# Kernel optimization log

Measured on AMD Instinct MI355X. Metric: run time of the kernel, lower is better.

Reference implementation:

```python
import jax, jax.numpy as jnp
import numpy as np
import math

L = 6          # num_layers
D = 512        # hidden_dim
S = 2048       # seq_len
B = 8          # batch
ODIM = 1       # output_dim
SCALES = (24.0, 720.0)


def setup_inputs() -> dict:
    key = jax.random.key(0)
    ks = jax.random.split(key, 12)
    def n(k, shape, scale=0.02):
        return jax.random.normal(k, shape, dtype=jnp.float32) * scale
    return {
        "z": jax.random.normal(ks[0], (B, S, 1), dtype=jnp.float32),
        "c": jax.random.normal(ks[1], (B, S, 1), dtype=jnp.float32),
        "enc_w": n(ks[2], (D, 2)), "enc_b": jnp.zeros((D,), jnp.float32),
        "beta": jnp.ones((L, len(SCALES)), jnp.float32),
        "wq": n(ks[3], (L, D, D)), "bq": jnp.zeros((L, D), jnp.float32),
        "wk": n(ks[4], (L, D, D)), "bk": jnp.zeros((L, D), jnp.float32),
        "wv": n(ks[5], (L, D, D)), "bv": jnp.zeros((L, D), jnp.float32),
        "ln1_w": jnp.ones((L, D), jnp.float32), "ln1_b": jnp.zeros((L, D), jnp.float32),
        "ln2_w": jnp.ones((L, D), jnp.float32), "ln2_b": jnp.zeros((L, D), jnp.float32),
        "ff1_w": n(ks[6], (L, 4 * D, D)), "ff1_b": jnp.zeros((L, 4 * D), jnp.float32),
        "ff2_w": n(ks[7], (L, D, 4 * D)), "ff2_b": jnp.zeros((L, D), jnp.float32),
        "out_w": n(ks[8], (ODIM, D)), "out_b": jnp.zeros((ODIM,), jnp.float32),
    }


def _ln(x, w, b, eps=1e-5):
    m = jnp.mean(x, axis=-1, keepdims=True)
    v = jnp.var(x, axis=-1, keepdims=True)
    return (x - m) * jax.lax.rsqrt(v + eps) * w + b


def _posenc(seq_len, dim):
    pos = jnp.arange(seq_len, dtype=jnp.float32)[:, None]
    div = jnp.exp(jnp.arange(0, dim, 2, dtype=jnp.float32) * (-(math.log(10000.0) / dim)))
    pe = jnp.zeros((seq_len, dim), jnp.float32)
    pe = pe.at[:, 0::2].set(jnp.sin(pos * div))
    pe = pe.at[:, 1::2].set(jnp.cos(pos * div))
    return pe


def reference(z, c, enc_w, enc_b, beta, wq, bq, wk, bk, wv, bv,
              ln1_w, ln1_b, ln2_w, ln2_b, ff1_w, ff1_b, ff2_w, ff2_b,
              out_w, out_b):
    # SequenceEncoder: cat(z,c) -> Linear(2, D) -> + sinusoidal PE
    x = jnp.concatenate([z, c], axis=-1) @ enc_w.T + enc_b       # [B,S,D]
    seq_len, d = x.shape[1], x.shape[2]
    x = x + _posenc(seq_len, d)[None]
    sqrt_d = math.sqrt(d)

    idx = jnp.arange(seq_len, dtype=jnp.float32)
    dist = jnp.abs(idx[:, None] - idx[None, :])                  # [S,S]

    for l in range(L):
        # pre-norm with ln1 (applied twice in the original code - replicated)
        xn = _ln(x, ln1_w[l], ln1_b[l])
        Q = xn @ wq[l].T + bq[l]
        K = xn @ wk[l].T + bk[l]
        V = xn @ wv[l].T + bv[l]
        attn = jnp.einsum('bid,bjd->bij', Q, K) / sqrt_d          # [B,S,S]
        bias = beta[l, 0] * jnp.cos(2.0 * math.pi * dist / SCALES[0]) \
             + beta[l, 1] * jnp.cos(2.0 * math.pi * dist / SCALES[1])
        probs = jax.nn.softmax(attn + bias, axis=-1)
        att_out = jnp.einsum('bij,bjd->bid', probs, V)
        # original applies layer_norm_1 again to the residual sum
        x = _ln(x + att_out, ln1_w[l], ln1_b[l])
        xn2 = _ln(x, ln2_w[l], ln2_b[l])
        h = jax.nn.relu(xn2 @ ff1_w[l].T + ff1_b[l])
        x = x + h @ ff2_w[l].T + ff2_b[l]

    return x @ out_w.T + out_b                                    # [B,S,ODIM]
```

## Files before the change

### kernel.cpp

```cpp
#include <hip/hip_runtime.h>
#include <math.h>

#define BB 8
#define SS 2048
#define DD 512
#define LL 6
#define FFD 2048

typedef _Float16 half_t;
typedef __attribute__((ext_vector_type(8))) _Float16 half8;
typedef __attribute__((ext_vector_type(4))) _Float16 half4;
typedef __attribute__((ext_vector_type(4))) float f32x4;

enum { EPI_NONE = 0, EPI_RELU = 2, EPI_RES = 3, EPI_ATTN = 4, EPI_QKV = 5, EPI_PV = 6 };

__device__ __forceinline__ void gl_lds16(const void* g, void* l) {
    __builtin_amdgcn_global_load_lds(
        (const __attribute__((address_space(1))) unsigned int*)g,
        (__attribute__((address_space(3))) unsigned int*)l,
        16, 0, 0);
}

__device__ __forceinline__ void blockReduce2(float& a, float& b, float* sm) {
#pragma unroll
    for (int off = 32; off; off >>= 1) {
        a += __shfl_down(a, off);
        b += __shfl_down(b, off);
    }
    int lane = threadIdx.x & 63;
    int w = threadIdx.x >> 6;
    if (lane == 0) { sm[w] = a; sm[4 + w] = b; }
    __syncthreads();
    a = sm[0] + sm[1] + sm[2] + sm[3];
    b = sm[4] + sm[5] + sm[6] + sm[7];
    __syncthreads();
}

__global__ __launch_bounds__(256) void encode_kernel(
    const float* __restrict__ z, const float* __restrict__ c,
    const float* __restrict__ enc_w, const float* __restrict__ enc_b,
    float* __restrict__ x)
{
    int idx = blockIdx.x * 256 + threadIdx.x;
    int d  = idx & (DD - 1);
    int bs = idx >> 9;
    int s  = bs & (SS - 1);
    float v = z[bs] * enc_w[2 * d] + c[bs] * enc_w[2 * d + 1] + enc_b[d];
    float div = expf(-(float)(d & ~1) * (9.210340371976184f / 512.0f));
    float ang = (float)s * div;
    v += (d & 1) ? cosf(ang) : sinf(ang);
    x[idx] = v;
}

__global__ __launch_bounds__(256) void convert_layer_kernel(
    const float* __restrict__ wq, const float* __restrict__ wk,
    const float* __restrict__ wv, const float* __restrict__ f1,
    const float* __restrict__ f2, half_t* __restrict__ wqkv,
    half_t* __restrict__ f1h, half_t* __restrict__ f2h)
{
    const int NQ = DD * DD;
    int i = blockIdx.x * 256 + threadIdx.x;
    if (i < 3 * NQ) {
        int which = i >> 18, j = i & (NQ - 1);
        const float* s = (which == 0) ? wq : (which == 1) ? wk : wv;
        wqkv[i] = (half_t)s[j];
    } else {
        int k = i - 3 * NQ;
        if (k < FFD * DD) f1h[k] = (half_t)f1[k];
        else              f2h[k - FFD * DD] = (half_t)f2[k - FFD * DD];
    }
}

__global__ __launch_bounds__(256) void bias_table_kernel(
    const float* __restrict__ beta, float* __restrict__ tbl)
{
    int i = blockIdx.x * 256 + threadIdx.x;
    int l = i >> 11, d = i & (SS - 1);
    tbl[i] = beta[2 * l] * cosf(0.2617993877991494f * d)
           + beta[2 * l + 1] * cosf(0.008726646259971648f * d);
}

__global__ __launch_bounds__(256) void ln_kernel(
    const float* __restrict__ src, const float* __restrict__ w,
    const float* __restrict__ b, half_t* __restrict__ dst)
{
    __shared__ float sm[8];
    size_t row = blockIdx.x;
    const float* p = src + row * DD;
    int t = threadIdx.x;
    float v0 = p[t], v1 = p[t + 256];
    float s = v0 + v1, sq = v0 * v0 + v1 * v1;
    blockReduce2(s, sq, sm);
    float mean = s * (1.0f / DD);
    float var  = sq * (1.0f / DD) - mean * mean;
    float rs   = rsqrtf(var + 1e-5f);
    dst[row * DD + t]       = (half_t)((v0 - mean) * rs * w[t] + b[t]);
    dst[row * DD + t + 256] = (half_t)((v1 - mean) * rs * w[t + 256] + b[t + 256]);
}

__global__ __launch_bounds__(256) void add_ln_ln_kernel(
    float* __restrict__ x, const half_t* __restrict__ att,
    const float* __restrict__ w1, const float* __restrict__ b1,
    const float* __restrict__ w2, const float* __restrict__ b2,
    half_t* __restrict__ xn)
{
    __shared__ float sm[8];
    size_t row = blockIdx.x;
    int t = threadIdx.x;
    float v0 = x[row * DD + t] + (float)att[row * DD + t];
    float v1 = x[row * DD + t + 256] + (float)att[row * DD + t + 256];
    float s = v0 + v1, sq = v0 * v0 + v1 * v1;
    blockReduce2(s, sq, sm);
    float mean = s * (1.0f / DD);
    float var  = sq * (1.0f / DD) - mean * mean;
    float rs   = rsqrtf(var + 1e-5f);
    float y0 = (v0 - mean) * rs * w1[t] + b1[t];
    float y1 = (v1 - mean) * rs * w1[t + 256] + b1[t + 256];
    x[row * DD + t]       = y0;
    x[row * DD + t + 256] = y1;
    s = y0 + y1; sq = y0 * y0 + y1 * y1;
    blockReduce2(s, sq, sm);
    mean = s * (1.0f / DD);
    var  = sq * (1.0f / DD) - mean * mean;
    rs   = rsqrtf(var + 1e-5f);
    xn[row * DD + t]       = (half_t)((y0 - mean) * rs * w2[t] + b2[t]);
    xn[row * DD + t + 256] = (half_t)((y1 - mean) * rs * w2[t + 256] + b2[t + 256]);
}

template<int MT, int EPI, bool OHALF>
__global__ __launch_bounds__(256) void gemm_mfma(
    const half_t* __restrict__ A, const half_t* __restrict__ W,
    const float* __restrict__ bias, const float* __restrict__ res,
    void* __restrict__ Cp, int N, int K, float alpha,
    long long sA, long long sW, long long sC,
    const float* __restrict__ biasK, const float* __restrict__ biasV,
    half_t* __restrict__ Ck, half_t* __restrict__ Cv)
{
    constexpr int TM = MT / 32;
    constexpr int ABUF = MT * 32;
    constexpr int BBUF = 128 * 32;
    __shared__ __align__(16) half_t As[2 * ABUF];
    __shared__ __align__(16) half_t Bs[2 * BBUF];

    const int z = blockIdx.z;
    A += (size_t)z * sA; W += (size_t)z * sW;
    if (EPI == EPI_PV) res += (size_t)z * SS;
    float*  Cf = (float*)Cp  + (size_t)z * sC;
    half_t* Ch = (half_t*)Cp + (size_t)z * sC;

    const int tid = threadIdx.x;
    const int wv = tid >> 6, ln = tid & 63;
    const int bm = blockIdx.x * MT, bn = blockIdx.y * 128;
    const int wm = (wv & 1) * (MT / 2), wn = (wv >> 1) * 64;

    const int srow = wv * 16 + (ln >> 2);
    const int scol = (ln & 3) * 8;
    const half_t* Ag = A + (size_t)(bm + srow) * K + scol;
    const half_t* Bg = W + (size_t)(bn + srow) * K + scol;

    f32x4 acc[TM][4] = {};
    const int lane15 = ln & 15, quad = ln >> 4;
    const int koff = quad * 8;
    const int nIter = K >> 5;

    {
        char* a = (char*)As + wv * 1024;
        char* b = (char*)Bs + wv * 1024;
        gl_lds16(Ag, a);
        if (MT == 128) gl_lds16(Ag + (size_t)64 * K, a + 4096);
        gl_lds16(Bg, b);
        gl_lds16(Bg + (size_t)64 * K, b + 4096);
    }
    __syncthreads();

    for (int it = 0; it < nIter; ++it) {
        const int cur = it & 1;
        if (it + 1 < nIter) {
            const int k1 = (it + 1) << 5;
            char* a = (char*)As + (cur ^ 1) * (ABUF * 2) + wv * 1024;
            char* b = (char*)Bs + (cur ^ 1) * (BBUF * 2) + wv * 1024;
            gl_lds16(Ag + k1, a);
            if (MT == 128) gl_lds16(Ag + (size_t)64 * K + k1, a + 4096);
            gl_lds16(Bg + k1, b);
            gl_lds16(Bg + (size_t)64 * K + k1, b + 4096);
        }

        const half_t* Ab = As + cur * ABUF;
        const half_t* Bb = Bs + cur * BBUF;
        half8 aF[TM], bF[4];
#pragma unroll
        for (int i = 0; i < TM; ++i)
            aF[i] = *(const half8*)&Ab[(wm + i * 16 + lane15) * 32 + koff];
#pragma unroll
        for (int j = 0; j < 4; ++j)
            bF[j] = *(const half8*)&Bb[(wn + j * 16 + lane15) * 32 + koff];
#pragma unroll
        for (int i = 0; i < TM; ++i)
#pragma unroll
            for (int j = 0; j < 4; ++j)
                acc[i][j] = __builtin_amdgcn_mfma_f32_16x16x32_f16(
                    aF[i], bF[j], acc[i][j], 0, 0, 0);

        __syncthreads();
    }

#pragma unroll
    for (int i = 0; i < TM; ++i) {
        const int m0 = bm + wm + i * 16 + quad * 4;
#pragma unroll
        for (int j = 0; j < 4; ++j) {
            const int gn = bn + wn + j * 16 + lane15;
            if (EPI == EPI_QKV) {
                const int seg = gn >> 9, nn = gn & (DD - 1);
                if (seg == 2) {
                    half4 pk;
#pragma unroll
                    for (int r = 0; r < 4; ++r)
                        pk[r] = (half_t)(acc[i][j][r] + biasV[nn]);
                    const int b = m0 >> 11, s0 = m0 & (SS - 1);
                    *(half4*)&Cv[((size_t)b * DD + nn) * SS + s0] = pk;
                } else {
                    const float bs = (seg == 0) ? bias[nn] : biasK[nn];
                    half_t* dst = (seg == 0) ? Ch : Ck;
#pragma unroll
                    for (int r = 0; r < 4; ++r)
                        dst[(size_t)(m0 + r) * DD + nn] = (half_t)(acc[i][j][r] + bs);
                }
            } else {
#pragma unroll
                for (int r = 0; r < 4; ++r) {
                    const int gm = m0 + r;
                    float v = acc[i][j][r];
                    if (EPI == EPI_ATTN) {
                        int dist = gm - gn; if (dist < 0) dist = -dist;
                        v = __expf(fminf(v * alpha + bias[dist], 10.0f));
                    } else if (EPI == EPI_PV) {
                        v *= res[gm];
                    } else {
                        if (EPI == EPI_RELU) v = fmaxf(v + bias[gn], 0.0f);
                        if (EPI == EPI_RES)  v += bias[gn] + res[(size_t)gm * N + gn];
                    }
                    if (OHALF) Ch[(size_t)gm * N + gn] = (half_t)v;
                    else       Cf[(size_t)gm * N + gn] = v;
                }
            }
        }
    }
}

__global__ __launch_bounds__(256) void rowsum_kernel(
    const half_t* __restrict__ sc, float* __restrict__ inv)
{
    int row = blockIdx.x * 4 + (threadIdx.x >> 6);
    int lane = threadIdx.x & 63;
    const half8* r = (const half8*)(sc + (size_t)row * SS);
    float s = 0.f;
#pragma unroll
    for (int k = 0; k < 4; ++k) {
        half8 v = r[lane + 64 * k];
#pragma unroll
        for (int i = 0; i < 8; ++i) s += (float)v[i];
    }
#pragma unroll
    for (int off = 32; off; off >>= 1) s += __shfl_down(s, off);
    if (lane == 0) inv[row] = 1.0f / s;
}

__global__ __launch_bounds__(256) void out_kernel(
    const float* __restrict__ x, const float* __restrict__ ow,
    const float* __restrict__ ob, float* __restrict__ out)
{
    int row = blockIdx.x * 4 + (threadIdx.x >> 6);
    int lane = threadIdx.x & 63;
    const float* p = x + (size_t)row * DD;
    float s = 0.f;
#pragma unroll
    for (int k = 0; k < 8; ++k) s += p[lane + 64 * k] * ow[lane + 64 * k];
#pragma unroll
    for (int off = 32; off; off >>= 1) s += __shfl_down(s, off);
    if (lane == 0) out[row] = s + ob[0];
}

extern "C" void kernel_launch(void* const* d_in, const int* in_sizes, int n_in,
                              void* d_out, int out_size, void* d_ws, size_t ws_size,
                              hipStream_t stream)
{
    (void)in_sizes; (void)n_in; (void)out_size; (void)ws_size;
    const float* z     = (const float*)d_in[0];
    const float* c     = (const float*)d_in[1];
    const float* enc_w = (const float*)d_in[2];
    const float* enc_b = (const float*)d_in[3];
    const float* beta  = (const float*)d_in[4];
    const float* wq    = (const float*)d_in[5];
    const float* bq    = (const float*)d_in[6];
    const float* wk    = (const float*)d_in[7];
    const float* bk    = (const float*)d_in[8];
    const float* wv    = (const float*)d_in[9];
    const float* bv    = (const float*)d_in[10];
    const float* ln1w  = (const float*)d_in[11];
    const float* ln1b  = (const float*)d_in[12];
    const float* ln2w  = (const float*)d_in[13];
    const float* ln2b  = (const float*)d_in[14];
    const float* ff1w  = (const float*)d_in[15];
    const float* ff1b  = (const float*)d_in[16];
    const float* ff2w  = (const float*)d_in[17];
    const float* ff2b  = (const float*)d_in[18];
    const float* ow    = (const float*)d_in[19];
    const float* ob    = (const float*)d_in[20];

    const size_t BSD = (size_t)BB * SS * DD;
    const size_t BSS = (size_t)BB * SS * SS;

    char* p = (char*)d_ws;
    float*  x    = (float*)p;  p += BSD * 4;
    half_t* xnh  = (half_t*)p; p += BSD * 2;
    half_t* sch  = (half_t*)p; p += BSS * 2;
    char*   pool = p;          p += BSD * 2 * 4;
    half_t* atth = (half_t*)pool;
    half_t* qh   = (half_t*)(pool + BSD * 2);
    half_t* kh   = (half_t*)(pool + BSD * 4);
    half_t* vth  = (half_t*)(pool + BSD * 6);
    half_t* hh   = (half_t*)pool;
    half_t* wqkv = (half_t*)p; p += (size_t)3 * DD * DD * 2;
    half_t* f1h  = (half_t*)p; p += (size_t)FFD * DD * 2;
    half_t* f2h  = (half_t*)p; p += (size_t)FFD * DD * 2;
    float*  tbl  = (float*)p;  p += (size_t)LL * SS * 4;
    float*  sums = (float*)p;

    const float alpha = 0.044194173824159216f;
    const int BS = BB * SS;
    const long long sQ = (long long)SS * DD, sP = (long long)SS * SS,
                    sV = (long long)DD * SS;
    const int CONV_BLKS = (3 * DD * DD + 2 * FFD * DD) / 256;

    bias_table_kernel<<<LL * SS / 256, 256, 0, stream>>>(beta, tbl);
    encode_kernel<<<BS * DD / 256, 256, 0, stream>>>(z, c, enc_w, enc_b, x);

    for (int l = 0; l < LL; ++l) {
        convert_layer_kernel<<<CONV_BLKS, 256, 0, stream>>>(
            wq + (size_t)l * DD * DD, wk + (size_t)l * DD * DD,
            wv + (size_t)l * DD * DD, ff1w + (size_t)l * FFD * DD,
            ff2w + (size_t)l * DD * FFD, wqkv, f1h, f2h);

        ln_kernel<<<BS, 256, 0, stream>>>(x, ln1w + l * DD, ln1b + l * DD, xnh);

        gemm_mfma<128, EPI_QKV, true><<<dim3(BS / 128, 12, 1), 256, 0, stream>>>(
            xnh, wqkv, bq + l * DD, nullptr, qh, DD, DD, 0, 0, 0, 0,
            bk + l * DD, bv + l * DD, kh, vth);

        gemm_mfma<128, EPI_ATTN, true><<<dim3(SS / 128, SS / 128, BB), 256, 0, stream>>>(
            qh, kh, tbl + l * SS, nullptr, sch, SS, DD, alpha, sQ, sQ, sP,
            nullptr, nullptr, nullptr, nullptr);

        rowsum_kernel<<<BS / 4, 256, 0, stream>>>(sch, sums);

        gemm_mfma<64, EPI_PV, true><<<dim3(SS / 64, DD / 128, BB), 256, 0, stream>>>(
            sch, vth, nullptr, sums, atth, DD, SS, 0, sP, sV, sQ,
            nullptr, nullptr, nullptr, nullptr);

        add_ln_ln_kernel<<<BS, 256, 0, stream>>>(x, atth, ln1w + l * DD, ln1b + l * DD,
                                                 ln2w + l * DD, ln2b + l * DD, xnh);

        gemm_mfma<128, EPI_RELU, true><<<dim3(BS / 128, FFD / 128, 1), 256, 0, stream>>>(
            xnh, f1h, ff1b + l * FFD, nullptr, hh, FFD, DD, 0, 0, 0, 0,
            nullptr, nullptr, nullptr, nullptr);
        gemm_mfma<64, EPI_RES, false><<<dim3(BS / 64, DD / 128, 1), 256, 0, stream>>>(
            hh, f2h, ff2b + l * DD, x, x, DD, FFD, 0, 0, 0, 0,
            nullptr, nullptr, nullptr, nullptr);
    }

    out_kernel<<<BS / 4, 256, 0, stream>>>(x, ow, ob, (float*)d_out);
}
```

Measured before the change: 2.039 ms.

## Fuse softmax row-sum into PV GEMM and swizzle attention-score block order

Removes the separate rowsum kernel by accumulating row sums of the fp16 score tiles from the A fragments already loaded inside the PV GEMM, reducing them across lanes with shuffles and scaling the output by the reciprocal. This saves a full extra read of the BxSxS score matrix per layer and one launch. The attention-score GEMM also switches to a 1D grid with a swizzled block-index mapping that groups tiles for better L2 reuse of Q/K. The fused sum adds some VALU conversion work to the PV inner loop.

```diff
diff --git a/kernel.cpp b/kernel.cpp
--- a/kernel.cpp
+++ b/kernel.cpp
@@ -127,7 +127,7 @@
     xn[row * DD + t + 256] = (half_t)((y1 - mean) * rs * w2[t + 256] + b2[t + 256]);
 }
 
-template<int MT, int EPI, bool OHALF>
+template<int MT, int EPI, bool OHALF, int SWZ = 0>
 __global__ __launch_bounds__(256) void gemm_mfma(
     const half_t* __restrict__ A, const half_t* __restrict__ W,
     const float* __restrict__ bias, const float* __restrict__ res,
@@ -142,15 +142,23 @@
     __shared__ __align__(16) half_t As[2 * ABUF];
     __shared__ __align__(16) half_t Bs[2 * BBUF];
 
-    const int z = blockIdx.z;
+    int bxi, byi, bzi;
+    if (SWZ == 1) {
+        const int id = blockIdx.x;
+        const int cc = id & 7, rr = id >> 3;
+        bxi = rr & 15;
+        const int ss = cc + 8 * (rr >> 4);
+        byi = ss & 15; bzi = ss >> 4;
+    } else { bxi = blockIdx.x; byi = blockIdx.y; bzi = blockIdx.z; }
+
+    const int z = bzi;
     A += (size_t)z * sA; W += (size_t)z * sW;
-    if (EPI == EPI_PV) res += (size_t)z * SS;
     float*  Cf = (float*)Cp  + (size_t)z * sC;
     half_t* Ch = (half_t*)Cp + (size_t)z * sC;
 
     const int tid = threadIdx.x;
     const int wv = tid >> 6, ln = tid & 63;
-    const int bm = blockIdx.x * MT, bn = blockIdx.y * 128;
+    const int bm = bxi * MT, bn = byi * 128;
     const int wm = (wv & 1) * (MT / 2), wn = (wv >> 1) * 64;
 
     const int srow = wv * 16 + (ln >> 2);
@@ -159,6 +167,10 @@
     const half_t* Bg = W + (size_t)(bn + srow) * K + scol;
 
     f32x4 acc[TM][4] = {};
+    float rs[TM];
+#pragma unroll
+    for (int i = 0; i < TM; ++i) rs[i] = 0.f;
+
     const int lane15 = ln & 15, quad = ln >> 4;
     const int koff = quad * 8;
     const int nIter = K >> 5;
@@ -194,6 +206,14 @@
 #pragma unroll
         for (int j = 0; j < 4; ++j)
             bF[j] = *(const half8*)&Bb[(wn + j * 16 + lane15) * 32 + koff];
+
+        if (EPI == EPI_PV) {
+#pragma unroll
+            for (int i = 0; i < TM; ++i)
+#pragma unroll
+                for (int e = 0; e < 8; ++e) rs[i] += (float)aF[i][e];
+        }
+
 #pragma unroll
         for (int i = 0; i < TM; ++i)
 #pragma unroll
@@ -202,6 +222,19 @@
                     aF[i], bF[j], acc[i][j], 0, 0, 0);
 
         __syncthreads();
+    }
+
+    float inv[TM][4];
+    if (EPI == EPI_PV) {
+#pragma unroll
+        for (int i = 0; i < TM; ++i) {
+            rs[i] += __shfl_xor(rs[i], 16);
+            rs[i] += __shfl_xor(rs[i], 32);
+            rs[i] = 1.0f / rs[i];
+#pragma unroll
+            for (int r = 0; r < 4; ++r)
+                inv[i][r] = __shfl(rs[i], quad * 4 + r);
+        }
     }
 
 #pragma unroll
@@ -235,7 +268,7 @@
                         int dist = gm - gn; if (dist < 0) dist = -dist;
                         v = __expf(fminf(v * alpha + bias[dist], 10.0f));
                     } else if (EPI == EPI_PV) {
-                        v *= res[gm];
+                        v *= inv[i][r];
                     } else {
                         if (EPI == EPI_RELU) v = fmaxf(v + bias[gn], 0.0f);
                         if (EPI == EPI_RES)  v += bias[gn] + res[(size_t)gm * N + gn];
@@ -246,24 +279,6 @@
             }
         }
     }
-}
-
-__global__ __launch_bounds__(256) void rowsum_kernel(
-    const half_t* __restrict__ sc, float* __restrict__ inv)
-{
-    int row = blockIdx.x * 4 + (threadIdx.x >> 6);
-    int lane = threadIdx.x & 63;
-    const half8* r = (const half8*)(sc + (size_t)row * SS);
-    float s = 0.f;
-#pragma unroll
-    for (int k = 0; k < 4; ++k) {
-        half8 v = r[lane + 64 * k];
-#pragma unroll
-        for (int i = 0; i < 8; ++i) s += (float)v[i];
-    }
-#pragma unroll
-    for (int off = 32; off; off >>= 1) s += __shfl_down(s, off);
-    if (lane == 0) inv[row] = 1.0f / s;
 }
 
 __global__ __launch_bounds__(256) void out_kernel(
@@ -324,8 +339,7 @@
     half_t* wqkv = (half_t*)p; p += (size_t)3 * DD * DD * 2;
     half_t* f1h  = (half_t*)p; p += (size_t)FFD * DD * 2;
     half_t* f2h  = (half_t*)p; p += (size_t)FFD * DD * 2;
-    float*  tbl  = (float*)p;  p += (size_t)LL * SS * 4;
-    float*  sums = (float*)p;
+    float*  tbl  = (float*)p;
 
     const float alpha = 0.044194173824159216f;
     const int BS = BB * SS;
@@ -348,14 +362,12 @@
             xnh, wqkv, bq + l * DD, nullptr, qh, DD, DD, 0, 0, 0, 0,
             bk + l * DD, bv + l * DD, kh, vth);
 
-        gemm_mfma<128, EPI_ATTN, true><<<dim3(SS / 128, SS / 128, BB), 256, 0, stream>>>(
+        gemm_mfma<128, EPI_ATTN, true, 1><<<dim3(2048, 1, 1), 256, 0, stream>>>(
             qh, kh, tbl + l * SS, nullptr, sch, SS, DD, alpha, sQ, sQ, sP,
             nullptr, nullptr, nullptr, nullptr);
 
-        rowsum_kernel<<<BS / 4, 256, 0, stream>>>(sch, sums);
-
         gemm_mfma<64, EPI_PV, true><<<dim3(SS / 64, DD / 128, BB), 256, 0, stream>>>(
-            sch, vth, nullptr, sums, atth, DD, SS, 0, sP, sV, sQ,
+            sch, vth, nullptr, nullptr, atth, DD, SS, 0, sP, sV, sQ,
             nullptr, nullptr, nullptr, nullptr);
 
         add_ln_ln_kernel<<<BS, 256, 0, stream>>>(x, atth, ln1w + l * DD, ln1b + l * DD,
```

New measurement: 1.976 ms. 1.03x faster.
